# Performance work log

Hardware: AMD Instinct MI355X
Metric: run time of the kernel (lower is better)

## Reference

```python
import jax, jax.numpy as jnp
import numpy as np
from jax import lax
from jax.scipy.special import logsumexp

B, T, H, L = 64, 512, 768, 9


def setup_inputs() -> dict:
    key = jax.random.key(0)
    k1, k2, k3, k4, k5 = jax.random.split(key, 5)
    hidden = jax.random.normal(k1, (B, T, H), dtype=jnp.float32)
    W = jax.random.normal(k2, (L, H), dtype=jnp.float32) * 0.02
    b = jnp.zeros((L,), dtype=jnp.float32)
    transitions = jax.random.normal(k3, (L, L), dtype=jnp.float32) * 0.1
    lengths = jax.random.randint(k4, (B,), T // 2, T + 1)
    seq_mask = jnp.arange(T)[None, :] < lengths[:, None]          # [B,T] bool
    labels = jax.random.randint(k5, (B, T), 0, L).astype(jnp.int32)
    labels = jnp.where(seq_mask, labels, -100).astype(jnp.int32)   # -100 = ignore
    attention_mask = seq_mask.astype(jnp.int32)
    return {"hidden": hidden, "W": W, "b": b, "transitions": transitions,
            "labels": labels, "attention_mask": attention_mask}


def _crf_nll(logits, tags, transitions, mask):
    # numerator: joint score of the gold path (no start/end transitions)
    maskf = mask.astype(logits.dtype)
    emit = jnp.take_along_axis(logits, tags[..., None], axis=2)[..., 0]   # [B,T]
    emit_score = (emit * maskf).sum(-1)
    trans = transitions[tags[:, :-1], tags[:, 1:]]                        # [B,T-1]
    trans_score = (trans * maskf[:, 1:]).sum(-1)
    numerator = emit_score + trans_score
    # denominator: forward algorithm (log-sum-exp recurrence over time)
    def step(alpha, xs):
        logit_t, mask_t = xs                                   # [B,L], [B]
        inner = alpha[:, :, None] + transitions[None, :, :] + logit_t[:, None, :]
        new = logsumexp(inner, axis=1)
        return jnp.where(mask_t[:, None], new, alpha), None
    alpha0 = logits[:, 0]                                      # mask[:,0] assumed True
    alpha, _ = lax.scan(step, alpha0,
                        (jnp.transpose(logits[:, 1:], (1, 0, 2)), mask[:, 1:].T))
    denominator = logsumexp(alpha, axis=-1)
    return -(numerator - denominator).sum()


def _viterbi(logits, transitions, mask):
    num_tags = transitions.shape[0]
    identity_bp = jnp.broadcast_to(jnp.arange(num_tags)[None, :], logits.shape[:1] + (num_tags,))

    def vstep(vscore, xs):
        logit_t, mask_t = xs
        inner = vscore[:, :, None] + transitions[None, :, :]   # [B,L_prev,L_cur]
        bp = jnp.argmax(inner, axis=1)                         # [B,L]
        new = jnp.max(inner, axis=1) + logit_t
        vscore = jnp.where(mask_t[:, None], new, vscore)
        bp = jnp.where(mask_t[:, None], bp, identity_bp)       # carry tag through pad
        return vscore, bp

    vscore0 = logits[:, 0]
    vscore, bps = lax.scan(vstep, vscore0,
                           (jnp.transpose(logits[:, 1:], (1, 0, 2)), mask[:, 1:].T))
    last_tag = jnp.argmax(vscore, axis=-1)                     # [B]

    def btstep(tag, bp_t):
        prev = jnp.take_along_axis(bp_t, tag[:, None], axis=1)[:, 0]
        return prev, tag

    first_tag, tags_rest = lax.scan(btstep, last_tag, bps, reverse=True)  # ys[t]=tag_{t+1}
    return jnp.concatenate([first_tag[:, None], tags_rest.T], axis=1)     # [B,T]


def reference(hidden, W, b, transitions, labels, attention_mask):
    mask = (attention_mask != 0) & (labels != -100)            # create_combined_mask
    logits = jnp.einsum('bth,lh->btl', hidden, W) + b          # classifier (dropout=eval)
    tags = jnp.where(labels == -100, 0, labels)                # adjust_labels_for_crf
    loss = _crf_nll(logits, tags, transitions, mask)           # -log_likelihood (summed)
    vtags = _viterbi(logits, transitions, mask)                # [B,T]
    # pad_predictions: prepend -100, shift right, -100 outside the masked span
    bsz = hidden.shape[0]
    neg = jnp.full((bsz, 1), -100, dtype=jnp.int32)
    shifted = jnp.concatenate([neg, vtags[:, :-1].astype(jnp.int32)], axis=1)
    valid = jnp.concatenate([jnp.zeros((bsz, 1), bool), mask[:, :-1]], axis=1)
    predictions = jnp.where(valid, shifted, -100)
    return loss, predictions
```

## Files before the change

kernel.cpp:

```cpp
#include <hip/hip_runtime.h>

#define BATCH 64
#define TLEN  512
#define HDIM  768
#define LTAGS 9

#define WS_LOGD 0
#define WS_VM   2359296
#define WS_AM   5013504
#define WS_NUM  5677056

__global__ __launch_bounds__(256) void logits_kernel(
    const float* __restrict__ hidden, const float* __restrict__ W,
    const float* __restrict__ bvec, double* __restrict__ logitsD)
{
    __shared__ float sW[LTAGS * HDIM];
    __shared__ float sb[LTAGS];
    const int tid = threadIdx.x;
    for (int i = tid; i < LTAGS * HDIM; i += 256) sW[i] = W[i];
    if (tid < LTAGS) sb[tid] = bvec[tid];
    __syncthreads();

    const int lane = tid & 63;
    const int wave = tid >> 6;
    const int sub  = lane & 7;
    const int rg   = lane >> 3;

    const int rowBase = blockIdx.x * 64 + wave * 16;
    const int r0 = rowBase + rg;
    const int r1 = rowBase + rg + 8;
    const float* h0p = hidden + (size_t)r0 * HDIM;
    const float* h1p = hidden + (size_t)r1 * HDIM;

    double acc0[LTAGS], acc1[LTAGS];
    #pragma unroll
    for (int l = 0; l < LTAGS; ++l) { acc0[l] = 0.0; acc1[l] = 0.0; }

    #pragma unroll 2
    for (int i = 0; i < 24; ++i) {
        const int off = i * 32 + sub * 4;
        const float4 h0 = *(const float4*)(h0p + off);
        const float4 h1 = *(const float4*)(h1p + off);
        #pragma unroll
        for (int l = 0; l < LTAGS; ++l) {
            const float4 w = *(const float4*)&sW[l * HDIM + off];
            float d0 = h0.x * w.x;
            d0 = fmaf(h0.y, w.y, d0); d0 = fmaf(h0.z, w.z, d0); d0 = fmaf(h0.w, w.w, d0);
            float d1 = h1.x * w.x;
            d1 = fmaf(h1.y, w.y, d1); d1 = fmaf(h1.z, w.z, d1); d1 = fmaf(h1.w, w.w, d1);
            acc0[l] += (double)d0;
            acc1[l] += (double)d1;
        }
    }
    #pragma unroll
    for (int l = 0; l < LTAGS; ++l) {
        double v0 = acc0[l], v1 = acc1[l];
        #pragma unroll
        for (int off = 4; off > 0; off >>= 1) {
            v0 += __shfl_down(v0, off);
            v1 += __shfl_down(v1, off);
        }
        acc0[l] = v0; acc1[l] = v1;
    }
    if (sub == 0) {
        #pragma unroll
        for (int l = 0; l < LTAGS; ++l) {
            logitsD[(size_t)r0 * LTAGS + l] = acc0[l] + (double)sb[l];
            logitsD[(size_t)r1 * LTAGS + l] = acc1[l] + (double)sb[l];
        }
    }
}

__global__ __launch_bounds__(256) void chunk_kernel(
    const float* __restrict__ trans, const int* __restrict__ labels,
    const int* __restrict__ att, const double* __restrict__ logitsD,
    double* __restrict__ wsVM, float* __restrict__ wsAM,
    double* __restrict__ wsNum, float* __restrict__ out)
{
    __shared__ __align__(16) double sT64[90];
    __shared__ __align__(16) float  sE32[108];
    const int tid = threadIdx.x;
    if (tid < 81) {
        const int k = tid / 9, j = tid - 9 * k;
        float tv = trans[tid];
        sT64[k * 10 + j] = (double)tv;
        sE32[k * 12 + j] = __expf(tv);
    }
    if (blockIdx.x == 0 && tid == 0) out[0] = 0.f;
    __syncthreads();

    const int blk = blockIdx.x;
    if (blk < 144) {
        const int gid = blk * 256 + tid;
        const int b   = gid / 576;
        const int rem = gid - b * 576;
        const int c   = rem / 9;
        const int i   = rem - c * 9;

        double M[LTAGS];
        #pragma unroll
        for (int j = 0; j < LTAGS; ++j) M[j] = (i == j) ? 0.0 : -1e300;

        const double* lrow = logitsD + ((size_t)b * TLEN + (c * 8 + 1)) * LTAGS;
        const int* lab = labels + b * TLEN;
        const int* am  = att + b * TLEN;
        const int t0 = c * 8 + 1;

        double lg[LTAGS], lgN[LTAGS];
        #pragma unroll
        for (int j = 0; j < LTAGS; ++j) lg[j] = lrow[j];
        bool mk = (am[t0] != 0) && (lab[t0] != -100);

        for (int s = 0; s < 8; ++s) {
            bool mkN = false;
            const int tn = t0 + s + 1;
            if (s < 7 && tn <= TLEN - 1) {
                const double* ln = lrow + (s + 1) * LTAGS;
                #pragma unroll
                for (int j = 0; j < LTAGS; ++j) lgN[j] = ln[j];
                mkN = (am[tn] != 0) && (lab[tn] != -100);
            }
            double nw[LTAGS];
            #pragma unroll
            for (int k = 0; k < LTAGS; ++k) {
                const double2* r = (const double2*)&sT64[k * 10];
                const double2 r01 = r[0], r23 = r[1], r45 = r[2], r67 = r[3];
                const double r8 = sT64[k * 10 + 8];
                const double mk64 = M[k];
                if (k == 0) {
                    nw[0] = mk64 + r01.x; nw[1] = mk64 + r01.y;
                    nw[2] = mk64 + r23.x; nw[3] = mk64 + r23.y;
                    nw[4] = mk64 + r45.x; nw[5] = mk64 + r45.y;
                    nw[6] = mk64 + r67.x; nw[7] = mk64 + r67.y;
                    nw[8] = mk64 + r8;
                } else {
                    nw[0] = fmax(nw[0], mk64 + r01.x); nw[1] = fmax(nw[1], mk64 + r01.y);
                    nw[2] = fmax(nw[2], mk64 + r23.x); nw[3] = fmax(nw[3], mk64 + r23.y);
                    nw[4] = fmax(nw[4], mk64 + r45.x); nw[5] = fmax(nw[5], mk64 + r45.y);
                    nw[6] = fmax(nw[6], mk64 + r67.x); nw[7] = fmax(nw[7], mk64 + r67.y);
                    nw[8] = fmax(nw[8], mk64 + r8);
                }
            }
            #pragma unroll
            for (int j = 0; j < LTAGS; ++j) {
                M[j] = mk ? (nw[j] + lg[j]) : M[j];
                lg[j] = lgN[j];
            }
            mk = mkN;
        }
        double* dst = wsVM + (((size_t)b * 64 + c) * LTAGS + i) * LTAGS;
        #pragma unroll
        for (int j = 0; j < LTAGS; ++j) dst[j] = M[j];
    } else if (blk < 216) {
        const int gid = (blk - 144) * 256 + tid;
        const int b   = gid / 288;
        const int rem = gid - b * 288;
        const int c   = rem / 9;
        const int i   = rem - c * 9;

        float M[LTAGS];
        #pragma unroll
        for (int j = 0; j < LTAGS; ++j) M[j] = (i == j) ? 0.f : -1e30f;

        const double* lrow = logitsD + ((size_t)b * TLEN + (c * 16 + 1)) * LTAGS;
        const int* lab = labels + b * TLEN;
        const int* am  = att + b * TLEN;
        const int t0 = c * 16 + 1;

        float lg[LTAGS], lgN[LTAGS];
        #pragma unroll
        for (int j = 0; j < LTAGS; ++j) lg[j] = (float)lrow[j];
        bool mk = (am[t0] != 0) && (lab[t0] != -100);

        for (int s = 0; s < 16; ++s) {
            bool mkN = false;
            const int tn = t0 + s + 1;
            if (s < 15 && tn <= TLEN - 1) {
                const double* ln = lrow + (s + 1) * LTAGS;
                #pragma unroll
                for (int j = 0; j < LTAGS; ++j) lgN[j] = (float)ln[j];
                mkN = (am[tn] != 0) && (lab[tn] != -100);
            }
            float m = M[0];
            #pragma unroll
            for (int k = 1; k < LTAGS; ++k) m = fmaxf(m, M[k]);
            float P[LTAGS];
            #pragma unroll
            for (int k = 0; k < LTAGS; ++k) P[k] = __expf(M[k] - m);
            float sa[LTAGS];
            #pragma unroll
            for (int k = 0; k < LTAGS; ++k) {
                const float4* r = (const float4*)&sE32[k * 12];
                const float4 f03 = r[0], f47 = r[1];
                const float f8 = sE32[k * 12 + 8];
                const float pk = P[k];
                if (k == 0) {
                    sa[0] = pk * f03.x; sa[1] = pk * f03.y; sa[2] = pk * f03.z; sa[3] = pk * f03.w;
                    sa[4] = pk * f47.x; sa[5] = pk * f47.y; sa[6] = pk * f47.z; sa[7] = pk * f47.w;
                    sa[8] = pk * f8;
                } else {
                    sa[0] = fmaf(pk, f03.x, sa[0]); sa[1] = fmaf(pk, f03.y, sa[1]);
                    sa[2] = fmaf(pk, f03.z, sa[2]); sa[3] = fmaf(pk, f03.w, sa[3]);
                    sa[4] = fmaf(pk, f47.x, sa[4]); sa[5] = fmaf(pk, f47.y, sa[5]);
                    sa[6] = fmaf(pk, f47.z, sa[6]); sa[7] = fmaf(pk, f47.w, sa[7]);
                    sa[8] = fmaf(pk, f8,    sa[8]);
                }
            }
            #pragma unroll
            for (int j = 0; j < LTAGS; ++j) {
                float nwj = m + __logf(sa[j]) + lg[j];
                M[j] = mk ? nwj : M[j];
                lg[j] = lgN[j];
            }
            mk = mkN;
        }
        float* dst = wsAM + (((size_t)b * 32 + c) * LTAGS + i) * LTAGS;
        #pragma unroll
        for (int j = 0; j < LTAGS; ++j) dst[j] = M[j];
    } else {
        const int bb   = (blk - 216) * 4 + (tid >> 6);
        const int lane = tid & 63;
        const int* lab = labels + bb * TLEN;
        const int* am  = att + bb * TLEN;
        const double* lrowb = logitsD + (size_t)bb * TLEN * LTAGS;
        double part = 0.0;
        #pragma unroll
        for (int k = 0; k < 8; ++k) {
            const int t = lane + k * 64;
            int lv = lab[t], av = am[t];
            bool mkc = (av != 0) && (lv != -100);
            int tg = (lv == -100) ? 0 : lv;
            if (mkc) part += lrowb[(size_t)t * LTAGS + tg];
            if (t < TLEN - 1) {
                int lv2 = lab[t + 1], av2 = am[t + 1];
                bool mk2 = (av2 != 0) && (lv2 != -100);
                int tg2 = (lv2 == -100) ? 0 : lv2;
                if (mk2) part += sT64[tg * 10 + tg2];
            }
        }
        #pragma unroll
        for (int off = 32; off > 0; off >>= 1) part += __shfl_down(part, off);
        if (lane == 0) wsNum[bb] = part;
    }
}

__global__ __launch_bounds__(128) void crf2_kernel(
    const float* __restrict__ trans, const int* __restrict__ labels,
    const int* __restrict__ att, const double* __restrict__ logitsD,
    const double* __restrict__ wsVM, const float* __restrict__ wsAM,
    const double* __restrict__ wsNum, float* __restrict__ out)
{
    __shared__ __align__(16) double sVM[64 * 81];
    __shared__ __align__(16) float  sAM[32 * 81];
    __shared__ double sVstart[65 * LTAGS];
    __shared__ unsigned long long sBPp[513];
    __shared__ int sTagB[65];
    __shared__ __align__(16) double sT64[90];
    __shared__ unsigned char sMk[513];
    __shared__ double sDen;
    __shared__ int sLast;

    const int b = blockIdx.x, tid = threadIdx.x;
    const int wave = tid >> 6, lane = tid & 63;
    const unsigned long long IDMAP = 0x876543210ull;

    const double2* gVM = (const double2*)(wsVM + (size_t)b * 64 * 81);
    double2* sVM2 = (double2*)sVM;
    for (int i = tid; i < 2592; i += 128) sVM2[i] = gVM[i];
    const float4* gAM = (const float4*)(wsAM + (size_t)b * 32 * 81);
    float4* sAM4 = (float4*)sAM;
    for (int i = tid; i < 648; i += 128) sAM4[i] = gAM[i];

    const int* lab = labels + b * TLEN;
    const int* am  = att + b * TLEN;
    for (int t = tid; t < TLEN; t += 128) {
        int lv = lab[t], av = am[t];
        sMk[t] = (av != 0 && lv != -100) ? 1 : 0;
    }
    if (tid == 0) sMk[TLEN] = 0;
    if (tid < 81) {
        const int k = tid / 9, j = tid - 9 * k;
        sT64[k * 10 + j] = (double)trans[tid];
    }
    __syncthreads();

    if (wave == 0) {
        const int j = (lane < LTAGS) ? lane : (LTAGS - 1);
        double v = logitsD[(size_t)b * TLEN * LTAGS + j];
        double Mc[LTAGS], Mn[LTAGS];
        #pragma unroll
        for (int i = 0; i < LTAGS; ++i) Mc[i] = sVM[i * LTAGS + j];
        for (int c = 0; c < 64; ++c) {
            if (c < 63) {
                #pragma unroll
                for (int i = 0; i < LTAGS; ++i) Mn[i] = sVM[(c + 1) * 81 + i * LTAGS + j];
            }
            if (lane < LTAGS) sVstart[c * LTAGS + j] = v;
            double g[LTAGS];
            #pragma unroll
            for (int i = 0; i < LTAGS; ++i) g[i] = __shfl(v, i);
            double a0 = g[0] + Mc[0], a1 = g[1] + Mc[1], a2 = g[2] + Mc[2];
            double a3 = g[3] + Mc[3], a4 = g[4] + Mc[4], a5 = g[5] + Mc[5];
            double a6 = g[6] + Mc[6], a7 = g[7] + Mc[7], a8 = g[8] + Mc[8];
            double t01 = fmax(a0, a1), t23 = fmax(a2, a3);
            double t45 = fmax(a4, a5), t67 = fmax(a6, a7);
            v = fmax(fmax(fmax(t01, t23), fmax(t45, t67)), a8);
            if (c < 63) {
                #pragma unroll
                for (int i = 0; i < LTAGS; ++i) Mc[i] = Mn[i];
            }
        }
        if (lane < LTAGS) sVstart[64 * LTAGS + j] = v;
        double g[LTAGS];
        #pragma unroll
        for (int i = 0; i < LTAGS; ++i) g[i] = __shfl(v, i);
        if (lane == 0) {
            int bi = 0; double bv = g[0];
            #pragma unroll
            for (int i = 1; i < LTAGS; ++i) if (g[i] > bv) { bv = g[i]; bi = i; }
            sLast = bi;
        }
    } else {
        const int j = (lane < LTAGS) ? lane : (LTAGS - 1);
        float v = (float)logitsD[(size_t)b * TLEN * LTAGS + j];
        float Mc[LTAGS], Mn[LTAGS];
        #pragma unroll
        for (int i = 0; i < LTAGS; ++i) Mc[i] = sAM[i * LTAGS + j];
        for (int c = 0; c < 32; ++c) {
            if (c < 31) {
                #pragma unroll
                for (int i = 0; i < LTAGS; ++i) Mn[i] = sAM[(c + 1) * 81 + i * LTAGS + j];
            }
            float g[LTAGS];
            #pragma unroll
            for (int i = 0; i < LTAGS; ++i) g[i] = __shfl(v, i);
            float a[LTAGS];
            #pragma unroll
            for (int i = 0; i < LTAGS; ++i) a[i] = g[i] + Mc[i];
            float t01 = fmaxf(a[0], a[1]), t23 = fmaxf(a[2], a[3]);
            float t45 = fmaxf(a[4], a[5]), t67 = fmaxf(a[6], a[7]);
            float m = fmaxf(fmaxf(fmaxf(t01, t23), fmaxf(t45, t67)), a[8]);
            float sacc = 0.f;
            #pragma unroll
            for (int i = 0; i < LTAGS; ++i) sacc += __expf(a[i] - m);
            v = m + __logf(sacc);
            if (c < 31) {
                #pragma unroll
                for (int i = 0; i < LTAGS; ++i) Mc[i] = Mn[i];
            }
        }
        float g[LTAGS];
        #pragma unroll
        for (int i = 0; i < LTAGS; ++i) g[i] = __shfl(v, i);
        if (lane == 0) {
            float m = g[0];
            #pragma unroll
            for (int i = 1; i < LTAGS; ++i) m = fmaxf(m, g[i]);
            float sacc = 0.f;
            #pragma unroll
            for (int i = 0; i < LTAGS; ++i) sacc += __expf(g[i] - m);
            sDen = (double)(m + __logf(sacc));
        }
    }
    __syncthreads();

    unsigned long long S = IDMAP;
    if (tid < 64) {
        const int c = tid;
        double v[LTAGS];
        #pragma unroll
        for (int j = 0; j < LTAGS; ++j) v[j] = sVstart[c * LTAGS + j];
        const double* lrow = logitsD + ((size_t)b * TLEN + (c * 8 + 1)) * LTAGS;
        double lg[LTAGS], lgN[LTAGS];
        #pragma unroll
        for (int j = 0; j < LTAGS; ++j) lg[j] = lrow[j];

        for (int s = 0; s < 8; ++s) {
            const int t = c * 8 + 1 + s;
            if (s < 7 && t + 1 <= TLEN - 1) {
                const double* ln = lrow + (s + 1) * LTAGS;
                #pragma unroll
                for (int j = 0; j < LTAGS; ++j) lgN[j] = ln[j];
            }
            const bool mk = (sMk[t] != 0);
            double bst[LTAGS];
            int bi[LTAGS];
            #pragma unroll
            for (int k = 0; k < LTAGS; ++k) {
                const double2* r = (const double2*)&sT64[k * 10];
                const double2 r01 = r[0], r23 = r[1], r45 = r[2], r67 = r[3];
                const double r8 = sT64[k * 10 + 8];
                const double vk = v[k];
                double cnd[LTAGS];
                cnd[0] = vk + r01.x; cnd[1] = vk + r01.y;
                cnd[2] = vk + r23.x; cnd[3] = vk + r23.y;
                cnd[4] = vk + r45.x; cnd[5] = vk + r45.y;
                cnd[6] = vk + r67.x; cnd[7] = vk + r67.y;
                cnd[8] = vk + r8;
                if (k == 0) {
                    #pragma unroll
                    for (int j = 0; j < LTAGS; ++j) { bst[j] = cnd[j]; bi[j] = 0; }
                } else {
                    #pragma unroll
                    for (int j = 0; j < LTAGS; ++j) {
                        bool gt = cnd[j] > bst[j];
                        bst[j] = gt ? cnd[j] : bst[j];
                        bi[j]  = gt ? k : bi[j];
                    }
                }
            }
            unsigned long long pk = 0;
            #pragma unroll
            for (int j = 0; j < LTAGS; ++j)
                pk |= ((unsigned long long)bi[j]) << (4 * j);
            pk = mk ? pk : IDMAP;
            sBPp[t] = pk;
            #pragma unroll
            for (int j = 0; j < LTAGS; ++j) {
                v[j] = mk ? (bst[j] + lg[j]) : v[j];
                lg[j] = lgN[j];
            }
        }
        unsigned long long G = IDMAP;
        for (int s = 7; s >= 0; --s) {
            const unsigned long long bp = sBPp[c * 8 + 1 + s];
            unsigned long long ng = 0;
            #pragma unroll
            for (int j = 0; j < LTAGS; ++j) {
                int gj = (int)((G >> (4 * j)) & 15);
                int f  = (int)((bp >> (4 * gj)) & 15);
                ng |= ((unsigned long long)f) << (4 * j);
            }
            G = ng;
        }
        S = G;
    }

    #pragma unroll
    for (int d = 1; d < 64; d <<= 1) {
        unsigned long long Sn = __shfl_down(S, d);
        if (wave == 0 && lane + d < 64) {
            unsigned long long R = 0;
            #pragma unroll
            for (int x = 0; x < LTAGS; ++x) {
                int y = (int)((Sn >> (4 * x)) & 15);
                int z = (int)((S >> (4 * y)) & 15);
                R |= ((unsigned long long)z) << (4 * x);
            }
            S = R;
        }
    }
    if (tid < 64) {
        const int lt = sLast;
        sTagB[tid] = (int)((S >> (4 * lt)) & 15);
        if (tid == 0) sTagB[64] = lt;
    }
    __syncthreads();

    if (tid < 64) {
        const int c = tid;
        int cur = sTagB[c + 1];
        float* po = out + 1 + b * TLEN;
        for (int s = 8; s >= 1; --s) {
            const int t = c * 8 + s;
            if (t < TLEN) {
                int nxt = (int)((sBPp[t] >> (4 * cur)) & 15);
                po[t] = sMk[t - 1] ? (float)nxt : -100.f;
                cur = nxt;
            }
        }
    }
    if (tid == 0) {
        out[1 + b * TLEN] = -100.f;
        atomicAdd(out, (float)(sDen - wsNum[b]));
    }
}

extern "C" void kernel_launch(void* const* d_in, const int* in_sizes, int n_in,
                              void* d_out, int out_size, void* d_ws, size_t ws_size,
                              hipStream_t stream)
{
    const float* hidden = (const float*)d_in[0];
    const float* W      = (const float*)d_in[1];
    const float* bvec   = (const float*)d_in[2];
    const float* trans  = (const float*)d_in[3];
    const int*   labels = (const int*)d_in[4];
    const int*   att    = (const int*)d_in[5];
    float* out = (float*)d_out;

    char* ws = (char*)d_ws;
    double* logitsD = (double*)(ws + WS_LOGD);
    double* wsVM    = (double*)(ws + WS_VM);
    float*  wsAM    = (float*)(ws + WS_AM);
    double* wsNum   = (double*)(ws + WS_NUM);

    logits_kernel<<<512, 256, 0, stream>>>(hidden, W, bvec, logitsD);
    chunk_kernel<<<232, 256, 0, stream>>>(trans, labels, att, logitsD,
                                          wsVM, wsAM, wsNum, out);
    crf2_kernel<<<BATCH, 128, 0, stream>>>(trans, labels, att, logitsD,
                                           wsVM, wsAM, wsNum, out);
}
```

Measured before the change: 219.2 us.

## Replace serial Viterbi chunk-start scan with two-level parallel max-plus prefix

The 64-step serial max-plus scan over chunk matrices in crf2_kernel becomes a two-level scheme. First, 72 threads compose groups of 8 chunk matrices into superchunk matrices. Then each lane scans the 8 superchunks and applies up to 7 intra-group matrices to get its own chunk start vector. The shared buffer is reused for both the superchunk matrices and the backpointers. The chunk-matrix workspace is padded to a stride of 10 for aligned double2 loads, and the forward logsumexp wave no longer waits behind the Viterbi wave's barrier. In exchange it adds a barrier and redundant per-lane work, and shifts the workspace offsets.

```diff
diff --git a/kernel.cpp b/kernel.cpp
--- a/kernel.cpp
+++ b/kernel.cpp
@@ -7,8 +7,8 @@
 
 #define WS_LOGD 0
 #define WS_VM   2359296
-#define WS_AM   5013504
-#define WS_NUM  5677056
+#define WS_AM   5308416
+#define WS_NUM  5971968
 
 __global__ __launch_bounds__(256) void logits_kernel(
     const float* __restrict__ hidden, const float* __restrict__ W,
@@ -148,7 +148,7 @@
             }
             mk = mkN;
         }
-        double* dst = wsVM + (((size_t)b * 64 + c) * LTAGS + i) * LTAGS;
+        double* dst = wsVM + ((size_t)b * 64 + c) * 90 + (size_t)i * 10;
         #pragma unroll
         for (int j = 0; j < LTAGS; ++j) dst[j] = M[j];
     } else if (blk < 216) {
@@ -250,24 +250,22 @@
     const double* __restrict__ wsVM, const float* __restrict__ wsAM,
     const double* __restrict__ wsNum, float* __restrict__ out)
 {
-    __shared__ __align__(16) double sVM[64 * 81];
+    __shared__ __align__(16) double sVM[64 * 90];
     __shared__ __align__(16) float  sAM[32 * 81];
-    __shared__ double sVstart[65 * LTAGS];
-    __shared__ unsigned long long sBPp[513];
-    __shared__ int sTagB[65];
+    __shared__ __align__(16) double sU[720];
     __shared__ __align__(16) double sT64[90];
     __shared__ unsigned char sMk[513];
+    __shared__ int sTagB[65];
     __shared__ double sDen;
-    __shared__ int sLast;
 
     const int b = blockIdx.x, tid = threadIdx.x;
     const int wave = tid >> 6, lane = tid & 63;
     const unsigned long long IDMAP = 0x876543210ull;
 
-    const double2* gVM = (const double2*)(wsVM + (size_t)b * 64 * 81);
+    const double2* gVM = (const double2*)(wsVM + (size_t)b * 5760);
     double2* sVM2 = (double2*)sVM;
-    for (int i = tid; i < 2592; i += 128) sVM2[i] = gVM[i];
-    const float4* gAM = (const float4*)(wsAM + (size_t)b * 32 * 81);
+    for (int i = tid; i < 2880; i += 128) sVM2[i] = gVM[i];
+    const float4* gAM = (const float4*)(wsAM + (size_t)b * 2592);
     float4* sAM4 = (float4*)sAM;
     for (int i = tid; i < 648; i += 128) sAM4[i] = gAM[i];
 
@@ -284,92 +282,122 @@
     }
     __syncthreads();
 
+    double* sSM = sU;
+    if (tid < 72) {
+        const int g = tid / 9, i = tid - 9 * g;
+        double P[LTAGS];
+        {
+            const double* row = &sVM[(g * 8) * 90 + i * 10];
+            #pragma unroll
+            for (int j = 0; j < LTAGS; ++j) P[j] = row[j];
+        }
+        for (int m = g * 8 + 1; m < g * 8 + 8; ++m) {
+            double np[LTAGS];
+            #pragma unroll
+            for (int k = 0; k < LTAGS; ++k) {
+                const double2* r = (const double2*)&sVM[m * 90 + k * 10];
+                const double2 r01 = r[0], r23 = r[1], r45 = r[2], r67 = r[3];
+                const double r8 = sVM[m * 90 + k * 10 + 8];
+                const double pk = P[k];
+                if (k == 0) {
+                    np[0] = pk + r01.x; np[1] = pk + r01.y;
+                    np[2] = pk + r23.x; np[3] = pk + r23.y;
+                    np[4] = pk + r45.x; np[5] = pk + r45.y;
+                    np[6] = pk + r67.x; np[7] = pk + r67.y;
+                    np[8] = pk + r8;
+                } else {
+                    np[0] = fmax(np[0], pk + r01.x); np[1] = fmax(np[1], pk + r01.y);
+                    np[2] = fmax(np[2], pk + r23.x); np[3] = fmax(np[3], pk + r23.y);
+                    np[4] = fmax(np[4], pk + r45.x); np[5] = fmax(np[5], pk + r45.y);
+                    np[6] = fmax(np[6], pk + r67.x); np[7] = fmax(np[7], pk + r67.y);
+                    np[8] = fmax(np[8], pk + r8);
+                }
+            }
+            #pragma unroll
+            for (int j = 0; j < LTAGS; ++j) P[j] = np[j];
+        }
+        double* dst = &sSM[g * 90 + i * 10];
+        #pragma unroll
+        for (int j = 0; j < LTAGS; ++j) dst[j] = P[j];
+    }
+    __syncthreads();
+
+    unsigned long long* sBPp = (unsigned long long*)sU;
+    unsigned long long S = IDMAP;
+    int lastTag = 0;
+
     if (wave == 0) {
-        const int j = (lane < LTAGS) ? lane : (LTAGS - 1);
-        double v = logitsD[(size_t)b * TLEN * LTAGS + j];
-        double Mc[LTAGS], Mn[LTAGS];
-        #pragma unroll
-        for (int i = 0; i < LTAGS; ++i) Mc[i] = sVM[i * LTAGS + j];
-        for (int c = 0; c < 64; ++c) {
-            if (c < 63) {
+        const int c = lane;
+        const int myg = c >> 3;
+        double v[LTAGS], vS[LTAGS];
+        #pragma unroll
+        for (int j = 0; j < LTAGS; ++j) v[j] = logitsD[(size_t)b * TLEN * LTAGS + j];
+
+        #pragma unroll
+        for (int g = 0; g < 8; ++g) {
+            if (g == myg) {
                 #pragma unroll
-                for (int i = 0; i < LTAGS; ++i) Mn[i] = sVM[(c + 1) * 81 + i * LTAGS + j];
-            }
-            if (lane < LTAGS) sVstart[c * LTAGS + j] = v;
-            double g[LTAGS];
-            #pragma unroll
-            for (int i = 0; i < LTAGS; ++i) g[i] = __shfl(v, i);
-            double a0 = g[0] + Mc[0], a1 = g[1] + Mc[1], a2 = g[2] + Mc[2];
-            double a3 = g[3] + Mc[3], a4 = g[4] + Mc[4], a5 = g[5] + Mc[5];
-            double a6 = g[6] + Mc[6], a7 = g[7] + Mc[7], a8 = g[8] + Mc[8];
-            double t01 = fmax(a0, a1), t23 = fmax(a2, a3);
-            double t45 = fmax(a4, a5), t67 = fmax(a6, a7);
-            v = fmax(fmax(fmax(t01, t23), fmax(t45, t67)), a8);
-            if (c < 63) {
-                #pragma unroll
-                for (int i = 0; i < LTAGS; ++i) Mc[i] = Mn[i];
-            }
-        }
-        if (lane < LTAGS) sVstart[64 * LTAGS + j] = v;
-        double g[LTAGS];
-        #pragma unroll
-        for (int i = 0; i < LTAGS; ++i) g[i] = __shfl(v, i);
-        if (lane == 0) {
-            int bi = 0; double bv = g[0];
-            #pragma unroll
-            for (int i = 1; i < LTAGS; ++i) if (g[i] > bv) { bv = g[i]; bi = i; }
-            sLast = bi;
-        }
-    } else {
-        const int j = (lane < LTAGS) ? lane : (LTAGS - 1);
-        float v = (float)logitsD[(size_t)b * TLEN * LTAGS + j];
-        float Mc[LTAGS], Mn[LTAGS];
-        #pragma unroll
-        for (int i = 0; i < LTAGS; ++i) Mc[i] = sAM[i * LTAGS + j];
-        for (int c = 0; c < 32; ++c) {
-            if (c < 31) {
-                #pragma unroll
-                for (int i = 0; i < LTAGS; ++i) Mn[i] = sAM[(c + 1) * 81 + i * LTAGS + j];
-            }
-            float g[LTAGS];
-            #pragma unroll
-            for (int i = 0; i < LTAGS; ++i) g[i] = __shfl(v, i);
-            float a[LTAGS];
-            #pragma unroll
-            for (int i = 0; i < LTAGS; ++i) a[i] = g[i] + Mc[i];
-            float t01 = fmaxf(a[0], a[1]), t23 = fmaxf(a[2], a[3]);
-            float t45 = fmaxf(a[4], a[5]), t67 = fmaxf(a[6], a[7]);
-            float m = fmaxf(fmaxf(fmaxf(t01, t23), fmaxf(t45, t67)), a[8]);
-            float sacc = 0.f;
-            #pragma unroll
-            for (int i = 0; i < LTAGS; ++i) sacc += __expf(a[i] - m);
-            v = m + __logf(sacc);
-            if (c < 31) {
-                #pragma unroll
-                for (int i = 0; i < LTAGS; ++i) Mc[i] = Mn[i];
-            }
-        }
-        float g[LTAGS];
-        #pragma unroll
-        for (int i = 0; i < LTAGS; ++i) g[i] = __shfl(v, i);
-        if (lane == 0) {
-            float m = g[0];
-            #pragma unroll
-            for (int i = 1; i < LTAGS; ++i) m = fmaxf(m, g[i]);
-            float sacc = 0.f;
-            #pragma unroll
-            for (int i = 0; i < LTAGS; ++i) sacc += __expf(g[i] - m);
-            sDen = (double)(m + __logf(sacc));
-        }
-    }
-    __syncthreads();
-
-    unsigned long long S = IDMAP;
-    if (tid < 64) {
-        const int c = tid;
-        double v[LTAGS];
-        #pragma unroll
-        for (int j = 0; j < LTAGS; ++j) v[j] = sVstart[c * LTAGS + j];
+                for (int j = 0; j < LTAGS; ++j) vS[j] = v[j];
+            }
+            double nv[LTAGS];
+            #pragma unroll
+            for (int k = 0; k < LTAGS; ++k) {
+                const double2* r = (const double2*)&sSM[g * 90 + k * 10];
+                const double2 r01 = r[0], r23 = r[1], r45 = r[2], r67 = r[3];
+                const double r8 = sSM[g * 90 + k * 10 + 8];
+                const double vk = v[k];
+                if (k == 0) {
+                    nv[0] = vk + r01.x; nv[1] = vk + r01.y;
+                    nv[2] = vk + r23.x; nv[3] = vk + r23.y;
+                    nv[4] = vk + r45.x; nv[5] = vk + r45.y;
+                    nv[6] = vk + r67.x; nv[7] = vk + r67.y;
+                    nv[8] = vk + r8;
+                } else {
+                    nv[0] = fmax(nv[0], vk + r01.x); nv[1] = fmax(nv[1], vk + r01.y);
+                    nv[2] = fmax(nv[2], vk + r23.x); nv[3] = fmax(nv[3], vk + r23.y);
+                    nv[4] = fmax(nv[4], vk + r45.x); nv[5] = fmax(nv[5], vk + r45.y);
+                    nv[6] = fmax(nv[6], vk + r67.x); nv[7] = fmax(nv[7], vk + r67.y);
+                    nv[8] = fmax(nv[8], vk + r8);
+                }
+            }
+            #pragma unroll
+            for (int j = 0; j < LTAGS; ++j) v[j] = nv[j];
+        }
+        {
+            int bi = 0; double bv = v[0];
+            #pragma unroll
+            for (int i = 1; i < LTAGS; ++i) if (v[i] > bv) { bv = v[i]; bi = i; }
+            lastTag = bi;
+        }
+
+        const int nCat = c & 7;
+        for (int it = 0; it < nCat; ++it) {
+            const int m = (c & ~7) + it;
+            double nv[LTAGS];
+            #pragma unroll
+            for (int k = 0; k < LTAGS; ++k) {
+                const double2* r = (const double2*)&sVM[m * 90 + k * 10];
+                const double2 r01 = r[0], r23 = r[1], r45 = r[2], r67 = r[3];
+                const double r8 = sVM[m * 90 + k * 10 + 8];
+                const double vk = vS[k];
+                if (k == 0) {
+                    nv[0] = vk + r01.x; nv[1] = vk + r01.y;
+                    nv[2] = vk + r23.x; nv[3] = vk + r23.y;
+                    nv[4] = vk + r45.x; nv[5] = vk + r45.y;
+                    nv[6] = vk + r67.x; nv[7] = vk + r67.y;
+                    nv[8] = vk + r8;
+                } else {
+                    nv[0] = fmax(nv[0], vk + r01.x); nv[1] = fmax(nv[1], vk + r01.y);
+                    nv[2] = fmax(nv[2], vk + r23.x); nv[3] = fmax(nv[3], vk + r23.y);
+                    nv[4] = fmax(nv[4], vk + r45.x); nv[5] = fmax(nv[5], vk + r45.y);
+                    nv[6] = fmax(nv[6], vk + r67.x); nv[7] = fmax(nv[7], vk + r67.y);
+                    nv[8] = fmax(nv[8], vk + r8);
+                }
+            }
+            #pragma unroll
+            for (int j = 0; j < LTAGS; ++j) vS[j] = nv[j];
+        }
+
         const double* lrow = logitsD + ((size_t)b * TLEN + (c * 8 + 1)) * LTAGS;
         double lg[LTAGS], lgN[LTAGS];
         #pragma unroll
@@ -390,7 +418,7 @@
                 const double2* r = (const double2*)&sT64[k * 10];
                 const double2 r01 = r[0], r23 = r[1], r45 = r[2], r67 = r[3];
                 const double r8 = sT64[k * 10 + 8];
-                const double vk = v[k];
+                const double vk = vS[k];
                 double cnd[LTAGS];
                 cnd[0] = vk + r01.x; cnd[1] = vk + r01.y;
                 cnd[2] = vk + r23.x; cnd[3] = vk + r23.y;
@@ -417,7 +445,7 @@
             sBPp[t] = pk;
             #pragma unroll
             for (int j = 0; j < LTAGS; ++j) {
-                v[j] = mk ? (bst[j] + lg[j]) : v[j];
+                vS[j] = mk ? (bst[j] + lg[j]) : vS[j];
                 lg[j] = lgN[j];
             }
         }
@@ -434,6 +462,47 @@
             G = ng;
         }
         S = G;
+    } else {
+        const int j = (lane < LTAGS) ? lane : (LTAGS - 1);
+        float v = (float)logitsD[(size_t)b * TLEN * LTAGS + j];
+        float Mc[LTAGS], Mn[LTAGS];
+        #pragma unroll
+        for (int i = 0; i < LTAGS; ++i) Mc[i] = sAM[i * LTAGS + j];
+        for (int c = 0; c < 32; ++c) {
+            if (c < 31) {
+                #pragma unroll
+                for (int i = 0; i < LTAGS; ++i) Mn[i] = sAM[(c + 1) * 81 + i * LTAGS + j];
+            }
+            float g[LTAGS];
+            #pragma unroll
+            for (int i = 0; i < LTAGS; ++i) g[i] = __shfl(v, i);
+            float a[LTAGS];
+            #pragma unroll
+            for (int i = 0; i < LTAGS; ++i) a[i] = g[i] + Mc[i];
+            float t01 = fmaxf(a[0], a[1]), t23 = fmaxf(a[2], a[3]);
+            float t45 = fmaxf(a[4], a[5]), t67 = fmaxf(a[6], a[7]);
+            float m = fmaxf(fmaxf(fmaxf(t01, t23), fmaxf(t45, t67)), a[8]);
+            float sacc = 0.f;
+            #pragma unroll
+            for (int i = 0; i < LTAGS; ++i) sacc += __expf(a[i] - m);
+            v = m + __logf(sacc);
+            if (c < 31) {
+                #pragma unroll
+                for (int i = 0; i < LTAGS; ++i) Mc[i] = Mn[i];
+            }
+        }
+        float g[LTAGS];
+        #pragma unroll
+        for (int i = 0; i < LTAGS; ++i) g[i] = __shfl(v, i);
+        if (lane == 0) {
+            float m = g[0];
+            #pragma unroll
+            for (int i = 1; i < LTAGS; ++i) m = fmaxf(m, g[i]);
+            float sacc = 0.f;
+            #pragma unroll
+            for (int i = 0; i < LTAGS; ++i) sacc += __expf(g[i] - m);
+            sDen = (double)(m + __logf(sacc));
+        }
     }
 
     #pragma unroll
@@ -450,10 +519,9 @@
             S = R;
         }
     }
-    if (tid < 64) {
-        const int lt = sLast;
-        sTagB[tid] = (int)((S >> (4 * lt)) & 15);
-        if (tid == 0) sTagB[64] = lt;
+    if (wave == 0) {
+        sTagB[tid] = (int)((S >> (4 * lastTag)) & 15);
+        if (tid == 0) sTagB[64] = lastTag;
     }
     __syncthreads();
 
```

Result: no change. 221.2 us (+0.9%).
